# Optimization experiments

Measured on AMD Instinct MI355X. Metric: run time of the kernel, lower is better.

The kernel has to match this reference:

```python
import jax, jax.numpy as jnp
import numpy as np

B, DIM, H, W = 8, 64, 64, 64
N_EMBED = 512
NNZ = 4          # num_nonzero OMP iterations
REG = 1e-7       # tiny Tikhonov term for the batched normal-equation solves


def batch_omp(X, D, S):
    """Batch OMP: for each signal pick S atoms greedily and solve LS on support.
    X: [N, d] signals, D: [d, K] dictionary with unit-norm atoms.
    Returns dense sparse code [N, K] with <= S nonzeros per row.
    Mathematically equivalent to the incremental-Cholesky Batch_OMP: at each
    step we solve G_II gamma = alpha0_I on the current support I.
    """
    N, K = X.shape[0], D.shape[1]
    G = D.T @ D                 # [K, K] Gram matrix (precomputed once)
    alpha0 = X @ D              # [N, K] initial correlations D^T x
    alpha = alpha0
    idx_cols = []
    gamma = None
    idx = None
    for k in range(S):          # static small loop over sparsity level
        j = jnp.argmax(jnp.abs(alpha), axis=1)                # [N] greedy atom
        idx_cols.append(j)
        idx = jnp.stack(idx_cols, axis=1)                     # [N, k+1]
        G_sub = G[idx[:, :, None], idx[:, None, :]]           # [N, k+1, k+1]
        rhs = jnp.take_along_axis(alpha0, idx, axis=1)        # [N, k+1]
        reg = REG * jnp.eye(k + 1, dtype=G.dtype)
        gamma = jnp.linalg.solve(G_sub + reg, rhs[..., None])[..., 0]  # [N, k+1]
        # residual correlations: alpha = alpha0 - G[:, I] gamma  (G symmetric)
        alpha = alpha0 - jnp.einsum('nak,na->nk', G[idx], gamma)
    code = jnp.zeros((N, K), X.dtype).at[jnp.arange(N)[:, None], idx].set(gamma)
    return code


def setup_inputs() -> dict:
    key = jax.random.key(0)
    kx, kd = jax.random.split(key)
    x = jax.random.normal(kx, (B, DIM, H, W), dtype=jnp.float32)
    dictionary = jax.random.normal(kd, (DIM, N_EMBED), dtype=jnp.float32)
    return {"x": x, "dictionary": dictionary}


def reference(x, dictionary):
    perm = jnp.transpose(x, (0, 2, 3, 1))            # [B, H, W, C]
    flat = perm.reshape(-1, DIM)                     # [N, C], N = B*H*W
    # normalize_dict=True: atoms normalized to unit L2 norm (in-place in torch)
    Dn = dictionary / jnp.linalg.norm(dictionary, axis=0, keepdims=True)
    code = batch_omp(flat, Dn, NNZ)                  # [N, K] (torch keeps [K, N])
    quant = (code @ Dn.T).reshape(perm.shape)        # reconstruction
    diff_enc = jnp.mean((quant - perm) ** 2)
    diff_dict = diff_enc                             # backward_dict=False branch
    # straight-through: perm + (quant - perm).detach() == quant in value
    out = jnp.transpose(quant, (0, 3, 1, 2))         # [B, C, H, W]
    ids = jnp.transpose(code.reshape(B, H, W, N_EMBED), (0, 3, 1, 2))  # [B, K, H, W]
    norm_0 = jnp.sum(code != 0, axis=1).astype(jnp.float32)  # L0 per signal, [N]
    num_steps = jnp.float32(NNZ)
    mean_D = jnp.mean(jnp.abs(Dn))
    mean_Z = jnp.mean(jnp.abs(code))
    norm_Z = jnp.mean(norm_0)
    topk_num = max(1, int(norm_0.shape[0] * 0.01))   # static: 327
    top_percentile = jnp.min(jax.lax.top_k(norm_0, topk_num)[0])
    num_zeros = jnp.sum(norm_0 == 0).astype(jnp.float32)
    return (out, diff_enc, diff_dict, ids, num_steps, mean_D, mean_Z,
            norm_Z, top_percentile, num_zeros)
```

## Files before the change

### kernel.cpp

```cpp
#include <hip/hip_runtime.h>
#include <cstdint>
#include <cstddef>

#define BQ 8
#define CDIM 64
#define HQ 64
#define WQ 64
#define KDIM 512
#define N_SIG 32768
#define S_NNZ 4

#define DIFF_ENC_OFF 2097152
#define DIFF_DICT_OFF 2097153
#define IDS_OFF 2097154
#define NUM_STEPS_OFF 18874370
#define MEAN_D_OFF 18874371
#define MEAN_Z_OFF 18874372
#define NORM_Z_OFF 18874373
#define TOP_PCT_OFF 18874374
#define NUM_ZEROS_OFF 18874375

#define WS_DN 16
#define WS_DNT 32784
#define WS_G 65552
#define WS_WG 327696
#define WS_WI 458768

__global__ __launch_bounds__(64) void k_zero_acc(float* ws) {
  int t = threadIdx.x;
  if (t < 16) ((unsigned int*)ws)[t] = 0u;
}

__global__ __launch_bounds__(256) void k_dict(const float* __restrict__ D,
                                              float* __restrict__ Dn,
                                              float* __restrict__ DnT,
                                              double* __restrict__ accs) {
  int k = blockIdx.x * 256 + threadIdx.x;
  float ss = 0.f;
  for (int c = 0; c < CDIM; ++c) {
    float v = D[c * KDIM + k];
    ss = fmaf(v, v, ss);
  }
  float nrm = sqrtf(ss);
  float sabs = 0.f;
  for (int c = 0; c < CDIM; ++c) {
    float v = D[c * KDIM + k] / nrm;
    Dn[c * KDIM + k] = v;
    DnT[k * CDIM + c] = v;
    sabs += fabsf(v);
  }
#pragma unroll
  for (int off = 32; off >= 1; off >>= 1) sabs += __shfl_xor(sabs, off);
  if ((threadIdx.x & 63) == 0) atomicAdd(&accs[0], (double)sabs);
}

__global__ __launch_bounds__(256) void k_gram(const float* __restrict__ Dn,
                                              float* __restrict__ G) {
  int g = blockIdx.x * 256 + threadIdx.x;
  int i = g >> 9, j = g & 511;
  float s = 0.f;
#pragma unroll 8
  for (int c = 0; c < CDIM; ++c) s = fmaf(Dn[c * KDIM + i], Dn[c * KDIM + j], s);
  G[(size_t)i * KDIM + j] = s;
}

__global__ __launch_bounds__(256) void k_alpha0(const float* __restrict__ X,
                                                const float* __restrict__ Dn,
                                                float* __restrict__ A0) {
  __shared__ float Xs[64 * 65];
  __shared__ float Dns[64 * 64];
  int tid = threadIdx.x;
  int mt = blockIdx.x >> 3, nt = blockIdx.x & 7;
  int b = mt >> 6, h = mt & 63;
  int w = tid & 63, cq = tid >> 6;
#pragma unroll
  for (int p = 0; p < 16; ++p) {
    int c = p * 4 + cq;
    Xs[w * 65 + c] = X[(((size_t)b * CDIM + c) * HQ + h) * WQ + w];
    Dns[c * 64 + w] = Dn[(size_t)c * KDIM + nt * 64 + w];
  }
  __syncthreads();
  int ty = tid >> 4, tx = tid & 15;
  float acc[4][4] = {};
  for (int c = 0; c < 64; ++c) {
    float av[4];
#pragma unroll
    for (int i = 0; i < 4; ++i) av[i] = Xs[(ty * 4 + i) * 65 + c];
    float4 bv = *(const float4*)&Dns[c * 64 + tx * 4];
#pragma unroll
    for (int i = 0; i < 4; ++i) {
      acc[i][0] = fmaf(av[i], bv.x, acc[i][0]);
      acc[i][1] = fmaf(av[i], bv.y, acc[i][1]);
      acc[i][2] = fmaf(av[i], bv.z, acc[i][2]);
      acc[i][3] = fmaf(av[i], bv.w, acc[i][3]);
    }
  }
  size_t n0 = (size_t)mt * 64;
#pragma unroll
  for (int i = 0; i < 4; ++i) {
    float4 st = make_float4(acc[i][0], acc[i][1], acc[i][2], acc[i][3]);
    *(float4*)&A0[(n0 + ty * 4 + i) * KDIM + nt * 64 + tx * 4] = st;
  }
}

__device__ __forceinline__ float wave_get(const float (&v)[8], int k) {
  int src = k >> 3, m = k & 7;
  float x = v[0];
#pragma unroll
  for (int mm = 1; mm < 8; ++mm)
    if (m == mm) x = v[mm];
  return __shfl(x, src);
}

template <int SZ>
__device__ __forceinline__ void solve_sz(const float (&gs)[4][4], const float (&rhs)[4],
                                         float (&gamma)[4]) {
  double M[SZ][SZ];
  double y[SZ];
#pragma unroll
  for (int a = 0; a < SZ; ++a) {
    y[a] = (double)rhs[a];
#pragma unroll
    for (int b = 0; b < SZ; ++b) M[a][b] = (double)gs[a][b] + (a == b ? 1e-7 : 0.0);
  }
#pragma unroll
  for (int p = 0; p < SZ; ++p) {
    double inv = 1.0 / M[p][p];
#pragma unroll
    for (int r = p + 1; r < SZ; ++r) {
      double f = M[r][p] * inv;
#pragma unroll
      for (int c = p; c < SZ; ++c) M[r][c] -= f * M[p][c];
      y[r] -= f * y[p];
    }
  }
#pragma unroll
  for (int r = SZ - 1; r >= 0; --r) {
    double t = y[r];
#pragma unroll
    for (int c = r + 1; c < SZ; ++c) t -= M[r][c] * (double)gamma[c];
    gamma[r] = (float)(t / M[r][r]);
  }
}

template <int K>
__device__ __forceinline__ void omp_step(int lane, const float* __restrict__ G,
                                         float (&a0)[8], float (&al)[8], float (&Grow)[4][8],
                                         float (&gs)[4][4], float (&rhs)[4], int (&idx)[4],
                                         float (&gamma)[4]) {
  float bv = -1.0f;
  int bk = 0;
#pragma unroll
  for (int m = 0; m < 8; ++m) {
    float v = fabsf(al[m]);
    int ke = lane * 8 + m;
    if (v > bv) { bv = v; bk = ke; }
  }
#pragma unroll
  for (int off = 32; off >= 1; off >>= 1) {
    float ov = __shfl_xor(bv, off);
    int ok = __shfl_xor(bk, off);
    if (ov > bv || (ov == bv && ok < bk)) { bv = ov; bk = ok; }
  }
  idx[K] = bk;
  const float4* gp = (const float4*)(G + (size_t)bk * KDIM + lane * 8);
  float4 r0 = gp[0], r1 = gp[1];
  Grow[K][0] = r0.x; Grow[K][1] = r0.y; Grow[K][2] = r0.z; Grow[K][3] = r0.w;
  Grow[K][4] = r1.x; Grow[K][5] = r1.y; Grow[K][6] = r1.z; Grow[K][7] = r1.w;
#pragma unroll
  for (int b = 0; b < K; ++b) {
    float v = wave_get(Grow[K], idx[b]);
    gs[K][b] = v;
    gs[b][K] = v;
  }
  gs[K][K] = wave_get(Grow[K], idx[K]);
  rhs[K] = wave_get(a0, idx[K]);
  solve_sz<K + 1>(gs, rhs, gamma);
  if (K < 3) {
#pragma unroll
    for (int m = 0; m < 8; ++m) {
      float acc = a0[m];
#pragma unroll
      for (int a = 0; a <= K; ++a) acc = fmaf(-gamma[a], Grow[a][m], acc);
      al[m] = acc;
    }
  }
}

__global__ __launch_bounds__(256) void k_omp(const float* __restrict__ A0,
                                             const float* __restrict__ G,
                                             float4* __restrict__ wg, int4* __restrict__ wi) {
  int tid = threadIdx.x;
  int lane = tid & 63, wv = tid >> 6;
  int n = blockIdx.x * 4 + wv;
  const float4* ap = (const float4*)(A0 + (size_t)n * KDIM + lane * 8);
  float4 v0 = ap[0], v1 = ap[1];
  float a0[8] = {v0.x, v0.y, v0.z, v0.w, v1.x, v1.y, v1.z, v1.w};
  float al[8];
#pragma unroll
  for (int m = 0; m < 8; ++m) al[m] = a0[m];
  float Grow[4][8];
  float gs[4][4];
  float rhs[4];
  int idx[4];
  float gamma[4];
  omp_step<0>(lane, G, a0, al, Grow, gs, rhs, idx, gamma);
  omp_step<1>(lane, G, a0, al, Grow, gs, rhs, idx, gamma);
  omp_step<2>(lane, G, a0, al, Grow, gs, rhs, idx, gamma);
  omp_step<3>(lane, G, a0, al, Grow, gs, rhs, idx, gamma);
  if (lane == 0) {
    wg[n] = make_float4(gamma[0], gamma[1], gamma[2], gamma[3]);
    wi[n] = make_int4(idx[0], idx[1], idx[2], idx[3]);
  }
}

__global__ __launch_bounds__(256) void k_epi(const float* __restrict__ X,
                                             const float* __restrict__ DnT,
                                             const float4* __restrict__ wg,
                                             const int4* __restrict__ wi,
                                             float* __restrict__ out, double* __restrict__ accs,
                                             int* __restrict__ hist) {
  __shared__ int sIdx[64][4];
  __shared__ float sKg[64][4];
  __shared__ float q[64 * 65];
  __shared__ float red[4];
  int tid = threadIdx.x;
  int bh = blockIdx.x;
  int b = bh >> 6, h = bh & 63;

  if (tid < 64) {
    int w = tid;
    int n = bh * 64 + w;
    int4 iv = wi[n];
    float4 gv = wg[n];
    bool k0 = (iv.x != iv.y) && (iv.x != iv.z) && (iv.x != iv.w);
    bool k1 = (iv.y != iv.z) && (iv.y != iv.w);
    bool k2 = (iv.z != iv.w);
    float g0 = k0 ? gv.x : 0.f;
    float g1 = k1 ? gv.y : 0.f;
    float g2 = k2 ? gv.z : 0.f;
    float g3 = gv.w;
    sIdx[w][0] = iv.x; sIdx[w][1] = iv.y; sIdx[w][2] = iv.z; sIdx[w][3] = iv.w;
    sKg[w][0] = g0; sKg[w][1] = g1; sKg[w][2] = g2; sKg[w][3] = g3;
    int nz = (int)(k0 && gv.x != 0.f) + (int)(k1 && gv.y != 0.f) +
             (int)(k2 && gv.z != 0.f) + (int)(gv.w != 0.f);
    float sabs = (k0 ? fabsf(gv.x) : 0.f) + (k1 ? fabsf(gv.y) : 0.f) +
                 (k2 ? fabsf(gv.z) : 0.f) + fabsf(gv.w);
    float s = sabs;
#pragma unroll
    for (int off = 32; off >= 1; off >>= 1) s += __shfl_xor(s, off);
#pragma unroll
    for (int v = 0; v < 5; ++v) {
      unsigned long long m = __ballot(nz == v);
      if (tid == 0) {
        int c = (int)__popcll(m);
        if (c) atomicAdd(&hist[v], c);
      }
    }
    if (tid == 0) atomicAdd(&accs[1], (double)s);
  }
  __syncthreads();

  int w2 = tid & 63, p = tid >> 6, c0 = p * 16;
  float acc[16] = {};
#pragma unroll
  for (int s = 0; s < 4; ++s) {
    int ks = sIdx[w2][s];
    float g = sKg[w2][s];
    const float4* dp = (const float4*)(DnT + (size_t)ks * CDIM + c0);
#pragma unroll
    for (int i4 = 0; i4 < 4; ++i4) {
      float4 d = dp[i4];
      acc[i4 * 4 + 0] = fmaf(g, d.x, acc[i4 * 4 + 0]);
      acc[i4 * 4 + 1] = fmaf(g, d.y, acc[i4 * 4 + 1]);
      acc[i4 * 4 + 2] = fmaf(g, d.z, acc[i4 * 4 + 2]);
      acc[i4 * 4 + 3] = fmaf(g, d.w, acc[i4 * 4 + 3]);
    }
  }
#pragma unroll
  for (int i = 0; i < 16; ++i) q[(c0 + i) * 65 + w2] = acc[i];
  __syncthreads();

  float sumsq = 0.f;
#pragma unroll
  for (int pass = 0; pass < 16; ++pass) {
    int c = pass * 4 + p;
    float qv = q[c * 65 + w2];
    size_t off = (((size_t)b * CDIM + c) * HQ + h) * WQ + w2;
    float xv = X[off];
    float d = qv - xv;
    sumsq = fmaf(d, d, sumsq);
    out[off] = qv;
  }

  {
    int i0 = sIdx[w2][0], i1 = sIdx[w2][1], i2 = sIdx[w2][2], i3 = sIdx[w2][3];
    float g0 = sKg[w2][0], g1 = sKg[w2][1], g2 = sKg[w2][2], g3 = sKg[w2][3];
    float* ids = out + IDS_OFF;
    for (int kk = 0; kk < 128; ++kk) {
      int k = kk * 4 + p;
      float v = 0.f;
      v = (k == i0) ? g0 : v;
      v = (k == i1) ? g1 : v;
      v = (k == i2) ? g2 : v;
      v = (k == i3) ? g3 : v;
      ids[(((size_t)b * KDIM + k) * HQ + h) * WQ + w2] = v;
    }
  }

#pragma unroll
  for (int off = 32; off >= 1; off >>= 1) sumsq += __shfl_xor(sumsq, off);
  if ((tid & 63) == 0) red[tid >> 6] = sumsq;
  __syncthreads();
  if (tid == 0) atomicAdd(&accs[2], (double)(red[0] + red[1] + red[2] + red[3]));
}

__global__ __launch_bounds__(64) void k_final(const double* __restrict__ accs,
                                              const int* __restrict__ hist,
                                              float* __restrict__ out) {
  if (threadIdx.x == 0) {
    double sumAbsD = accs[0], sumAbsZ = accs[1], sumSq = accs[2];
    float diff = (float)(sumSq / 2097152.0);
    out[DIFF_ENC_OFF] = diff;
    out[DIFF_DICT_OFF] = diff;
    out[NUM_STEPS_OFF] = 4.0f;
    out[MEAN_D_OFF] = (float)(sumAbsD / 32768.0);
    out[MEAN_Z_OFF] = (float)(sumAbsZ / 16777216.0);
    int h0 = hist[0], h1 = hist[1], h2 = hist[2], h3 = hist[3], h4 = hist[4];
    out[NORM_Z_OFF] = (float)((double)(h1 + 2 * h2 + 3 * h3 + 4 * h4) / 32768.0);
    int cum = 0, res = 0;
    for (int v = 4; v >= 0; --v) {
      cum += hist[v];
      if (cum >= 327) { res = v; break; }
    }
    out[TOP_PCT_OFF] = (float)res;
    out[NUM_ZEROS_OFF] = (float)h0;
  }
}

extern "C" void kernel_launch(void* const* d_in, const int* in_sizes, int n_in,
                              void* d_out, int out_size, void* d_ws, size_t ws_size,
                              hipStream_t stream) {
  (void)in_sizes; (void)n_in; (void)out_size; (void)ws_size;
  const float* X = (const float*)d_in[0];
  const float* D = (const float*)d_in[1];
  float* out = (float*)d_out;
  float* W = (float*)d_ws;
  double* accs = (double*)d_ws;
  int* hist = (int*)W + 8;
  float* Dn = W + WS_DN;
  float* DnT = W + WS_DNT;
  float* G = W + WS_G;
  float4* wgam = (float4*)(W + WS_WG);
  int4* widx = (int4*)(W + WS_WI);
  float* A0 = out;

  hipLaunchKernelGGL(k_zero_acc, dim3(1), dim3(64), 0, stream, W);
  hipLaunchKernelGGL(k_dict, dim3(2), dim3(256), 0, stream, D, Dn, DnT, accs);
  hipLaunchKernelGGL(k_gram, dim3(1024), dim3(256), 0, stream, Dn, G);
  hipLaunchKernelGGL(k_alpha0, dim3(4096), dim3(256), 0, stream, X, Dn, A0);
  hipLaunchKernelGGL(k_omp, dim3(8192), dim3(256), 0, stream, A0, G, wgam, widx);
  hipLaunchKernelGGL(k_epi, dim3(512), dim3(256), 0, stream, X, DnT, wgam, widx, out, accs, hist);
  hipLaunchKernelGGL(k_final, dim3(1), dim3(64), 0, stream, accs, hist, out);
}
```

Before: 204.8 us.

## Split ids scatter into own kernel, simplify OMP argmax and use fp32 solve

Removes the zeroing kernel by folding it into a single-block k_dict. The OMP argmax becomes a max-reduce plus ballot, and Gram and alpha0 entries are read straight from global memory instead of through shuffle selects. The small normal-equation solve moves from double to fp32 with a hardware reciprocal. Duplicate-index masking moves into k_omp, and the large ids tensor write moves out of the 512-block epilogue into a new 2048-block kernel for more parallelism. The fp32 solve with approximate reciprocal may reduce accuracy on ill-conditioned supports.

```diff
diff --git a/kernel.cpp b/kernel.cpp
--- a/kernel.cpp
+++ b/kernel.cpp
@@ -26,16 +26,15 @@
 #define WS_WG 327696
 #define WS_WI 458768
 
-__global__ __launch_bounds__(64) void k_zero_acc(float* ws) {
-  int t = threadIdx.x;
-  if (t < 16) ((unsigned int*)ws)[t] = 0u;
-}
-
-__global__ __launch_bounds__(256) void k_dict(const float* __restrict__ D,
+__global__ __launch_bounds__(512) void k_dict(const float* __restrict__ D,
                                               float* __restrict__ Dn,
                                               float* __restrict__ DnT,
-                                              double* __restrict__ accs) {
-  int k = blockIdx.x * 256 + threadIdx.x;
+                                              float* __restrict__ W) {
+  int tid = threadIdx.x;
+  if (tid < 16) ((unsigned int*)W)[tid] = 0u;
+  __syncthreads();
+  double* accs = (double*)W;
+  int k = tid;
   float ss = 0.f;
   for (int c = 0; c < CDIM; ++c) {
     float v = D[c * KDIM + k];
@@ -51,7 +50,7 @@
   }
 #pragma unroll
   for (int off = 32; off >= 1; off >>= 1) sabs += __shfl_xor(sabs, off);
-  if ((threadIdx.x & 63) == 0) atomicAdd(&accs[0], (double)sabs);
+  if ((tid & 63) == 0) atomicAdd(&accs[0], (double)sabs);
 }
 
 __global__ __launch_bounds__(256) void k_gram(const float* __restrict__ Dn,
@@ -103,79 +102,76 @@
   }
 }
 
-__device__ __forceinline__ float wave_get(const float (&v)[8], int k) {
-  int src = k >> 3, m = k & 7;
-  float x = v[0];
-#pragma unroll
-  for (int mm = 1; mm < 8; ++mm)
-    if (m == mm) x = v[mm];
-  return __shfl(x, src);
-}
-
 template <int SZ>
 __device__ __forceinline__ void solve_sz(const float (&gs)[4][4], const float (&rhs)[4],
                                          float (&gamma)[4]) {
-  double M[SZ][SZ];
-  double y[SZ];
+  float M[SZ][SZ];
+  float y[SZ];
+  float idg[SZ];
 #pragma unroll
   for (int a = 0; a < SZ; ++a) {
-    y[a] = (double)rhs[a];
-#pragma unroll
-    for (int b = 0; b < SZ; ++b) M[a][b] = (double)gs[a][b] + (a == b ? 1e-7 : 0.0);
+    y[a] = rhs[a];
+#pragma unroll
+    for (int b = 0; b < SZ; ++b) M[a][b] = gs[a][b] + (a == b ? 1e-7f : 0.0f);
   }
 #pragma unroll
   for (int p = 0; p < SZ; ++p) {
-    double inv = 1.0 / M[p][p];
+    float ip = __builtin_amdgcn_rcpf(M[p][p]);
+    idg[p] = ip;
 #pragma unroll
     for (int r = p + 1; r < SZ; ++r) {
-      double f = M[r][p] * inv;
-#pragma unroll
-      for (int c = p; c < SZ; ++c) M[r][c] -= f * M[p][c];
-      y[r] -= f * y[p];
+      float f = M[r][p] * ip;
+#pragma unroll
+      for (int c = p + 1; c < SZ; ++c) M[r][c] = fmaf(-f, M[p][c], M[r][c]);
+      y[r] = fmaf(-f, y[p], y[r]);
     }
   }
 #pragma unroll
   for (int r = SZ - 1; r >= 0; --r) {
-    double t = y[r];
-#pragma unroll
-    for (int c = r + 1; c < SZ; ++c) t -= M[r][c] * (double)gamma[c];
-    gamma[r] = (float)(t / M[r][r]);
+    float t = y[r];
+#pragma unroll
+    for (int c = r + 1; c < SZ; ++c) t = fmaf(-M[r][c], gamma[c], t);
+    gamma[r] = t * idg[r];
   }
 }
 
 template <int K>
-__device__ __forceinline__ void omp_step(int lane, const float* __restrict__ G,
+__device__ __forceinline__ void omp_step(int lane, int n, const float* __restrict__ G,
+                                         const float* __restrict__ A0,
                                          float (&a0)[8], float (&al)[8], float (&Grow)[4][8],
                                          float (&gs)[4][4], float (&rhs)[4], int (&idx)[4],
                                          float (&gamma)[4]) {
-  float bv = -1.0f;
-  int bk = 0;
-#pragma unroll
-  for (int m = 0; m < 8; ++m) {
-    float v = fabsf(al[m]);
-    int ke = lane * 8 + m;
-    if (v > bv) { bv = v; bk = ke; }
-  }
-#pragma unroll
-  for (int off = 32; off >= 1; off >>= 1) {
-    float ov = __shfl_xor(bv, off);
-    int ok = __shfl_xor(bk, off);
-    if (ov > bv || (ov == bv && ok < bk)) { bv = ov; bk = ok; }
-  }
-  idx[K] = bk;
-  const float4* gp = (const float4*)(G + (size_t)bk * KDIM + lane * 8);
+  float mx = fabsf(al[0]);
+#pragma unroll
+  for (int m = 1; m < 8; ++m) mx = fmaxf(mx, fabsf(al[m]));
+#pragma unroll
+  for (int off = 32; off >= 1; off >>= 1) mx = fmaxf(mx, __shfl_xor(mx, off));
+  int mmask = 0;
+#pragma unroll
+  for (int m = 0; m < 8; ++m) mmask |= (fabsf(al[m]) == mx) ? (1 << m) : 0;
+  unsigned long long ball = __ballot(mmask != 0);
+  int srcl = (int)__builtin_ctzll(ball);
+  int bm = __builtin_ctz((unsigned)__shfl(mmask, srcl) | 0x100u);
+  int sk = __builtin_amdgcn_readfirstlane(srcl * 8 + bm);
+  idx[K] = sk;
+
+  const float4* gp = (const float4*)(G + (size_t)sk * KDIM + lane * 8);
   float4 r0 = gp[0], r1 = gp[1];
   Grow[K][0] = r0.x; Grow[K][1] = r0.y; Grow[K][2] = r0.z; Grow[K][3] = r0.w;
   Grow[K][4] = r1.x; Grow[K][5] = r1.y; Grow[K][6] = r1.z; Grow[K][7] = r1.w;
+
+  const float* grow_base = G + (size_t)sk * KDIM;
 #pragma unroll
   for (int b = 0; b < K; ++b) {
-    float v = wave_get(Grow[K], idx[b]);
+    float v = grow_base[idx[b]];
     gs[K][b] = v;
     gs[b][K] = v;
   }
-  gs[K][K] = wave_get(Grow[K], idx[K]);
-  rhs[K] = wave_get(a0, idx[K]);
+  gs[K][K] = grow_base[sk];
+  rhs[K] = A0[(size_t)n * KDIM + sk];
+
   solve_sz<K + 1>(gs, rhs, gamma);
+
   if (K < 3) {
 #pragma unroll
     for (int m = 0; m < 8; ++m) {
@@ -191,7 +187,8 @@
                                              const float* __restrict__ G,
                                              float4* __restrict__ wg, int4* __restrict__ wi) {
   int tid = threadIdx.x;
-  int lane = tid & 63, wv = tid >> 6;
+  int lane = tid & 63;
+  int wv = __builtin_amdgcn_readfirstlane(tid >> 6);
   int n = blockIdx.x * 4 + wv;
   const float4* ap = (const float4*)(A0 + (size_t)n * KDIM + lane * 8);
   float4 v0 = ap[0], v1 = ap[1];
@@ -204,12 +201,16 @@
   float rhs[4];
   int idx[4];
   float gamma[4];
-  omp_step<0>(lane, G, a0, al, Grow, gs, rhs, idx, gamma);
-  omp_step<1>(lane, G, a0, al, Grow, gs, rhs, idx, gamma);
-  omp_step<2>(lane, G, a0, al, Grow, gs, rhs, idx, gamma);
-  omp_step<3>(lane, G, a0, al, Grow, gs, rhs, idx, gamma);
+  omp_step<0>(lane, n, G, A0, a0, al, Grow, gs, rhs, idx, gamma);
+  omp_step<1>(lane, n, G, A0, a0, al, Grow, gs, rhs, idx, gamma);
+  omp_step<2>(lane, n, G, A0, a0, al, Grow, gs, rhs, idx, gamma);
+  omp_step<3>(lane, n, G, A0, a0, al, Grow, gs, rhs, idx, gamma);
+  bool k0 = (idx[0] != idx[1]) && (idx[0] != idx[2]) && (idx[0] != idx[3]);
+  bool k1 = (idx[1] != idx[2]) && (idx[1] != idx[3]);
+  bool k2 = (idx[2] != idx[3]);
   if (lane == 0) {
-    wg[n] = make_float4(gamma[0], gamma[1], gamma[2], gamma[3]);
+    wg[n] = make_float4(k0 ? gamma[0] : 0.f, k1 ? gamma[1] : 0.f,
+                        k2 ? gamma[2] : 0.f, gamma[3]);
     wi[n] = make_int4(idx[0], idx[1], idx[2], idx[3]);
   }
 }
@@ -233,20 +234,11 @@
     int n = bh * 64 + w;
     int4 iv = wi[n];
     float4 gv = wg[n];
-    bool k0 = (iv.x != iv.y) && (iv.x != iv.z) && (iv.x != iv.w);
-    bool k1 = (iv.y != iv.z) && (iv.y != iv.w);
-    bool k2 = (iv.z != iv.w);
-    float g0 = k0 ? gv.x : 0.f;
-    float g1 = k1 ? gv.y : 0.f;
-    float g2 = k2 ? gv.z : 0.f;
-    float g3 = gv.w;
     sIdx[w][0] = iv.x; sIdx[w][1] = iv.y; sIdx[w][2] = iv.z; sIdx[w][3] = iv.w;
-    sKg[w][0] = g0; sKg[w][1] = g1; sKg[w][2] = g2; sKg[w][3] = g3;
-    int nz = (int)(k0 && gv.x != 0.f) + (int)(k1 && gv.y != 0.f) +
-             (int)(k2 && gv.z != 0.f) + (int)(gv.w != 0.f);
-    float sabs = (k0 ? fabsf(gv.x) : 0.f) + (k1 ? fabsf(gv.y) : 0.f) +
-                 (k2 ? fabsf(gv.z) : 0.f) + fabsf(gv.w);
-    float s = sabs;
+    sKg[w][0] = gv.x; sKg[w][1] = gv.y; sKg[w][2] = gv.z; sKg[w][3] = gv.w;
+    int nz = (int)(gv.x != 0.f) + (int)(gv.y != 0.f) +
+             (int)(gv.z != 0.f) + (int)(gv.w != 0.f);
+    float s = fabsf(gv.x) + fabsf(gv.y) + fabsf(gv.z) + fabsf(gv.w);
 #pragma unroll
     for (int off = 32; off >= 1; off >>= 1) s += __shfl_xor(s, off);
 #pragma unroll
@@ -293,26 +285,43 @@
     out[off] = qv;
   }
 
-  {
-    int i0 = sIdx[w2][0], i1 = sIdx[w2][1], i2 = sIdx[w2][2], i3 = sIdx[w2][3];
-    float g0 = sKg[w2][0], g1 = sKg[w2][1], g2 = sKg[w2][2], g3 = sKg[w2][3];
-    float* ids = out + IDS_OFF;
-    for (int kk = 0; kk < 128; ++kk) {
-      int k = kk * 4 + p;
-      float v = 0.f;
-      v = (k == i0) ? g0 : v;
-      v = (k == i1) ? g1 : v;
-      v = (k == i2) ? g2 : v;
-      v = (k == i3) ? g3 : v;
-      ids[(((size_t)b * KDIM + k) * HQ + h) * WQ + w2] = v;
-    }
-  }
-
 #pragma unroll
   for (int off = 32; off >= 1; off >>= 1) sumsq += __shfl_xor(sumsq, off);
   if ((tid & 63) == 0) red[tid >> 6] = sumsq;
   __syncthreads();
   if (tid == 0) atomicAdd(&accs[2], (double)(red[0] + red[1] + red[2] + red[3]));
+}
+
+__global__ __launch_bounds__(256) void k_ids(const float4* __restrict__ wg,
+                                             const int4* __restrict__ wi,
+                                             float* __restrict__ out) {
+  __shared__ int4 sIdx[64];
+  __shared__ float4 sKg[64];
+  int tid = threadIdx.x;
+  int bh = blockIdx.x >> 2, kq = blockIdx.x & 3;
+  int b = bh >> 6, h = bh & 63;
+  if (tid < 64) {
+    int n = bh * 64 + tid;
+    sIdx[tid] = wi[n];
+    sKg[tid] = wg[n];
+  }
+  __syncthreads();
+  int w = tid & 63, kp = tid >> 6;
+  int4 iv = sIdx[w];
+  float4 gv = sKg[w];
+  int k0 = kq * 128 + kp * 32;
+  float* ids = out + IDS_OFF;
+  size_t base = (((size_t)b * KDIM + k0) * HQ + h) * WQ + w;
+#pragma unroll
+  for (int kk = 0; kk < 32; ++kk) {
+    int k = k0 + kk;
+    float v = 0.f;
+    v = (k == iv.x) ? gv.x : v;
+    v = (k == iv.y) ? gv.y : v;
+    v = (k == iv.z) ? gv.z : v;
+    v = (k == iv.w) ? gv.w : v;
+    ids[base + (size_t)kk * HQ * WQ] = v;
+  }
 }
 
 __global__ __launch_bounds__(64) void k_final(const double* __restrict__ accs,
@@ -355,11 +364,11 @@
   int4* widx = (int4*)(W + WS_WI);
   float* A0 = out;
 
-  hipLaunchKernelGGL(k_zero_acc, dim3(1), dim3(64), 0, stream, W);
-  hipLaunchKernelGGL(k_dict, dim3(2), dim3(256), 0, stream, D, Dn, DnT, accs);
+  hipLaunchKernelGGL(k_dict, dim3(1), dim3(512), 0, stream, D, Dn, DnT, W);
   hipLaunchKernelGGL(k_gram, dim3(1024), dim3(256), 0, stream, Dn, G);
   hipLaunchKernelGGL(k_alpha0, dim3(4096), dim3(256), 0, stream, X, Dn, A0);
   hipLaunchKernelGGL(k_omp, dim3(8192), dim3(256), 0, stream, A0, G, wgam, widx);
   hipLaunchKernelGGL(k_epi, dim3(512), dim3(256), 0, stream, X, DnT, wgam, widx, out, accs, hist);
+  hipLaunchKernelGGL(k_ids, dim3(2048), dim3(256), 0, stream, wgam, widx, out);
   hipLaunchKernelGGL(k_final, dim3(1), dim3(64), 0, stream, accs, hist, out);
 }
```

Result: faster. 190.2 us (-7.1%).
